# Kernel optimization log

Measured on AMD Instinct MI355X. Metric: run time of the kernel, lower is better.

## Reference

```python
import jax, jax.numpy as jnp
import numpy as np

KEY_DIM = 512
VAL_DIM = 512
BATCH = 32768
MEMORY_MAX_NORM = 5.0
TTT_LR_SCALE = 0.005
EPS = 1e-8


def setup_inputs() -> dict:
    key = jax.random.key(0)
    k1, k2, k3, k4, k5 = jax.random.split(key, 5)
    k = jax.random.normal(k1, (BATCH, KEY_DIM), dtype=jnp.float32)
    v = jax.random.normal(k2, (BATCH, VAL_DIM), dtype=jnp.float32)
    # memory weight init: normal(std=0.01)
    mem_w = jax.random.normal(k3, (VAL_DIM, KEY_DIM), dtype=jnp.float32) * 0.01
    # gate_proj: init is zeros/0.5; use small random weight + 0.5 bias for a
    # non-degenerate but realistic post-warmup state
    gate_w = jax.random.normal(k4, (3, KEY_DIM + VAL_DIM), dtype=jnp.float32) * 0.01
    gate_b = jnp.full((3,), 0.5, dtype=jnp.float32)
    momentum_S = jax.random.normal(k5, (VAL_DIM, KEY_DIM), dtype=jnp.float32) * 0.01
    return {"k": k, "v": v, "mem_w": mem_w, "gate_w": gate_w,
            "gate_b": gate_b, "momentum_S": momentum_S}


def _norm_clip(x, max_norm):
    n = jnp.linalg.norm(x)
    return jnp.where(n > max_norm, x * (max_norm / (n + EPS)), x)


def reference(k, v, mem_w, gate_w, gate_b, momentum_S):
    # retrieve: M(k) = k @ W^T ; loss = MSE(pred, v)
    retrieved = k @ mem_w.T                      # [B, val_dim]
    diff = retrieved - v
    loss = jnp.mean(diff * diff)

    # gates from batch-mean key/value
    kv_agg = jnp.concatenate([k.mean(0), v.mean(0)], axis=-1)  # [key+val]
    gates = jax.nn.sigmoid(kv_agg @ gate_w.T + gate_b)         # [3]
    alpha, eta, theta = gates[0], gates[1], gates[2]

    # analytic grad of MSE wrt W: 2/(B*val_dim) * (pred - v)^T @ k
    B, vd = diff.shape
    grad = (2.0 / (B * vd)) * (diff.T @ k)       # [val_dim, key_dim]
    grad_c = jnp.clip(grad, -1.0, 1.0)

    new_momentum = eta * momentum_S - TTT_LR_SCALE * theta * grad_c
    new_momentum = _norm_clip(new_momentum, MEMORY_MAX_NORM)

    new_weight = (1.0 - alpha) * mem_w + new_momentum
    new_weight = _norm_clip(new_weight, MEMORY_MAX_NORM)

    return retrieved, loss, new_weight, new_momentum, alpha, eta, theta
```

## Files before the change

### kernel.cpp

```cpp
#include <hip/hip_runtime.h>
#include <math.h>


typedef __bf16 bf16x8 __attribute__((ext_vector_type(8)));
typedef float f32x4 __attribute__((ext_vector_type(4)));
typedef float float4_t __attribute__((ext_vector_type(4)));
typedef unsigned short ushort4_t __attribute__((ext_vector_type(4)));
typedef unsigned short ushort8_t __attribute__((ext_vector_type(8)));

#define OUT_LOSS   16777216
#define OUT_W      16777217
#define OUT_MOM    17039361
#define OUT_ALPHA  17301505

#define OFF_GRAD   0u
#define OFF_CKP    1048576u
#define OFF_CVP    1572864u
#define OFF_LOSSP  2097152u
#define OFF_COLK   2105344u
#define OFF_COLV   2107392u
#define OFF_SCAL   2109440u
#define OFF_W16    2109504u
#define OFF_K16    2633792u
#define OFF_DIFF   36188224u
#define OFF_MRAW   OFF_K16
#define OFF_WRAW   (OFF_K16 + 1048576u)

__device__ __forceinline__ ushort4_t cvt4(float4_t v) {
  union { __bf16 b; unsigned short u; } c0, c1, c2, c3;
  c0.b = (__bf16)v.x; c1.b = (__bf16)v.y; c2.b = (__bf16)v.z; c3.b = (__bf16)v.w;
  ushort4_t h; h.x = c0.u; h.y = c1.u; h.z = c2.u; h.w = c3.u;
  return h;
}

__device__ __forceinline__ void gload_lds16(const unsigned short* g, unsigned short* l) {
  __builtin_amdgcn_global_load_lds(
      (const __attribute__((address_space(1))) unsigned int*)g,
      (__attribute__((address_space(3))) unsigned int*)l, 16, 0, 0);
}

__global__ __launch_bounds__(256) void k1_convert(
    const float* __restrict__ Kp, const float* __restrict__ Wp,
    unsigned short* __restrict__ k16, unsigned short* __restrict__ w16,
    float* __restrict__ colk_part)
{
  __shared__ float cp[512];
  const int t = threadIdx.x;
  const int cg = t & 127;
  const int g = t >> 7;
  const int b = blockIdx.x;
  if (b < 256) {
    const int r0 = b << 7;
    float p0 = 0.f, p1 = 0.f, p2 = 0.f, p3 = 0.f;
#pragma unroll 4
    for (int rr = g; rr < 128; rr += 2) {
      const size_t off = (size_t)(r0 + rr) * 512 + (cg << 2);
      const float4_t v = *reinterpret_cast<const float4_t*>(&Kp[off]);
      *reinterpret_cast<ushort4_t*>(&k16[off]) = cvt4(v);
      p0 += v.x; p1 += v.y; p2 += v.z; p3 += v.w;
    }
    if (g == 1) {
      cp[(cg << 2) + 0] = p0; cp[(cg << 2) + 1] = p1;
      cp[(cg << 2) + 2] = p2; cp[(cg << 2) + 3] = p3;
    }
    __syncthreads();
    if (g == 0) {
      colk_part[(size_t)b * 512 + (cg << 2) + 0] = p0 + cp[(cg << 2) + 0];
      colk_part[(size_t)b * 512 + (cg << 2) + 1] = p1 + cp[(cg << 2) + 1];
      colk_part[(size_t)b * 512 + (cg << 2) + 2] = p2 + cp[(cg << 2) + 2];
      colk_part[(size_t)b * 512 + (cg << 2) + 3] = p3 + cp[(cg << 2) + 3];
    }
  } else {
    const int r0 = (b - 256) << 5;
#pragma unroll 4
    for (int rr = g; rr < 32; rr += 2) {
      const size_t off = (size_t)(r0 + rr) * 512 + (cg << 2);
      const float4_t v = *reinterpret_cast<const float4_t*>(&Wp[off]);
      *reinterpret_cast<ushort4_t*>(&w16[off]) = cvt4(v);
    }
  }
}

__global__ __launch_bounds__(256) void k2_gemm(
    const unsigned short* __restrict__ k16, const unsigned short* __restrict__ w16,
    const float* __restrict__ Vp, float* __restrict__ outp,
    unsigned short* __restrict__ diff16,
    float* __restrict__ colv_part, float* __restrict__ loss_part)
{
  __shared__ __align__(16) unsigned short As[8192];
  __shared__ __align__(16) unsigned short Bs[4096];
  __shared__ float redc[128];
  __shared__ float redl[4];

  const int t = threadIdx.x, lane = t & 63, wv = t >> 6;
  const int tile = (blockIdx.x & 7) * 256 + (blockIdx.x >> 3);
  const int rt = tile >> 3, vt = tile & 7;
  const int row0 = rt << 7, vd0 = vt << 6;

  f32x4 acc[4][2];
#pragma unroll
  for (int m = 0; m < 4; ++m)
#pragma unroll
    for (int n = 0; n < 2; ++n)
      acc[m][n] = (f32x4){0.f, 0.f, 0.f, 0.f};

  const int srow = (wv << 3) + (lane >> 3);
  const int scol = (lane & 7) << 3;
  const unsigned short* pA = k16 + (size_t)(row0 + srow) * 512 + scol;
  const unsigned short* pB = w16 + (size_t)(vd0 + srow) * 512 + scol;
  unsigned short* lA = &As[wv << 9];
  unsigned short* lB = &Bs[wv << 9];

  const int fr = lane & 15, fq = lane >> 4;
  const int wr = (wv >> 1) << 6, wc = (wv & 1) << 5;

  for (int kk0 = 0; kk0 < 512; kk0 += 64) {
#pragma unroll
    for (int i = 0; i < 4; ++i)
      gload_lds16(pA + (i << 14) + kk0, lA + (i << 11));
#pragma unroll
    for (int i = 0; i < 2; ++i)
      gload_lds16(pB + (i << 14) + kk0, lB + (i << 11));
    __syncthreads();
#pragma unroll
    for (int kk = 0; kk < 64; kk += 32) {
      const int co = kk + (fq << 3);
      bf16x8 af[4], bfv[2];
#pragma unroll
      for (int m = 0; m < 4; ++m)
        af[m] = *reinterpret_cast<const bf16x8*>(&As[((wr + (m << 4) + fr) << 6) + co]);
#pragma unroll
      for (int n = 0; n < 2; ++n)
        bfv[n] = *reinterpret_cast<const bf16x8*>(&Bs[((wc + (n << 4) + fr) << 6) + co]);
#pragma unroll
      for (int m = 0; m < 4; ++m)
#pragma unroll
        for (int n = 0; n < 2; ++n)
          acc[m][n] = __builtin_amdgcn_mfma_f32_16x16x32_bf16(af[m], bfv[n], acc[m][n], 0, 0, 0);
    }
    __syncthreads();
  }

  float lsum = 0.f;
  float vcs[2] = {0.f, 0.f};
#pragma unroll
  for (int m = 0; m < 4; ++m) {
#pragma unroll
    for (int n = 0; n < 2; ++n) {
#pragma unroll
      for (int i = 0; i < 4; ++i) {
        const int rl = wr + (m << 4) + (fq << 2) + i;
        const int cl = wc + (n << 4) + fr;
        const size_t oi = (size_t)(row0 + rl) * 512 + vd0 + cl;
        const float rv = acc[m][n][i];
        outp[oi] = rv;
        const float vv = Vp[oi];
        const float d = rv - vv;
        lsum += d * d;
        vcs[n] += vv;
        union { __bf16 b; unsigned short u; } cd; cd.b = (__bf16)d;
        diff16[oi] = cd.u;
      }
    }
  }
#pragma unroll
  for (int o = 32; o; o >>= 1) lsum += __shfl_xor(lsum, o);
  if (lane == 0) redl[wv] = lsum;
#pragma unroll
  for (int n = 0; n < 2; ++n) {
    vcs[n] += __shfl_xor(vcs[n], 16);
    vcs[n] += __shfl_xor(vcs[n], 32);
  }
  if (fq == 0) {
#pragma unroll
    for (int n = 0; n < 2; ++n)
      redc[(wv << 5) + (n << 4) + fr] = vcs[n];
  }
  __syncthreads();
  if (t < 64) {
    const int h = t >> 5, lc = t & 31;
    colv_part[(size_t)rt * 512 + vd0 + t] =
        redc[(h << 5) + lc] + redc[((h + 2) << 5) + lc];
  }
  if (t == 0)
    loss_part[tile] = redl[0] + redl[1] + redl[2] + redl[3];
}

__global__ __launch_bounds__(256) void k3_grad(
    const unsigned short* __restrict__ diff16,
    const unsigned short* __restrict__ k16,
    float* __restrict__ grad)
{
  __shared__ __align__(16) unsigned short At[2][128][40];
  __shared__ __align__(16) unsigned short Bt[2][128][40];
  const int t = threadIdx.x;
  const int lane = t & 63;
  const int wv = t >> 6;
  const int b = blockIdx.x;
  const int x = b & 7;
  const int q = b >> 3;
  const int tile = q & 15;
  const int kc = ((q >> 4) << 3) | x;
  const int vd0 = (tile & 3) << 7;
  const int kd0 = (tile >> 2) << 7;
  const size_t r0 = (size_t)kc << 10;

  f32x4 acc[4][4];
#pragma unroll
  for (int m = 0; m < 4; ++m)
#pragma unroll
    for (int n = 0; n < 4; ++n)
      acc[m][n] = (f32x4){0.f, 0.f, 0.f, 0.f};

  const int dr = t >> 3;
  const int c0 = (t & 7) << 4;
  const int wr = (wv >> 1) << 6;
  const int wc = (wv & 1) << 6;
  const int fr = lane & 15;
  const int fq = lane >> 4;

  int cur = 0;
  for (int rr = 0; rr < 1024; rr += 32) {
    const size_t rowoff = (r0 + rr + dr) << 9;
    const ushort8_t a0 = *reinterpret_cast<const ushort8_t*>(&diff16[rowoff + vd0 + c0]);
    const ushort8_t a1 = *reinterpret_cast<const ushort8_t*>(&diff16[rowoff + vd0 + c0 + 8]);
    const ushort8_t b0 = *reinterpret_cast<const ushort8_t*>(&k16[rowoff + kd0 + c0]);
    const ushort8_t b1 = *reinterpret_cast<const ushort8_t*>(&k16[rowoff + kd0 + c0 + 8]);
    const int swz = ((c0 >> 4) & 3) << 3;
#pragma unroll
    for (int j = 0; j < 8; ++j) {
      const int drs = dr ^ swz;
      At[cur][c0 + j][drs] = a0[j];
      At[cur][c0 + 8 + j][drs] = a1[j];
      Bt[cur][c0 + j][drs] = b0[j];
      Bt[cur][c0 + 8 + j][drs] = b1[j];
    }
    __syncthreads();
    bf16x8 af[4], bfv[4];
#pragma unroll
    for (int m = 0; m < 4; ++m) {
      const int rA = wr + (m << 4) + fr;
      af[m] = *reinterpret_cast<const bf16x8*>(&At[cur][rA][(fq ^ ((rA >> 4) & 3)) << 3]);
    }
#pragma unroll
    for (int n = 0; n < 4; ++n) {
      const int rB = wc + (n << 4) + fr;
      bfv[n] = *reinterpret_cast<const bf16x8*>(&Bt[cur][rB][(fq ^ ((rB >> 4) & 3)) << 3]);
    }
#pragma unroll
    for (int m = 0; m < 4; ++m)
#pragma unroll
      for (int n = 0; n < 4; ++n)
        acc[m][n] = __builtin_amdgcn_mfma_f32_16x16x32_bf16(af[m], bfv[n], acc[m][n], 0, 0, 0);
    cur ^= 1;
  }
#pragma unroll
  for (int m = 0; m < 4; ++m)
#pragma unroll
    for (int n = 0; n < 4; ++n)
#pragma unroll
      for (int i = 0; i < 4; ++i)
        atomicAdd(&grad[(size_t)(vd0 + wr + (m << 4) + (fq << 2) + i) * 512
                        + kd0 + wc + (n << 4) + fr], acc[m][n][i]);
}

__global__ __launch_bounds__(256) void c1a_redcols(
    const float* __restrict__ ckp, const float* __restrict__ cvp,
    float* __restrict__ colk, float* __restrict__ colv)
{
  __shared__ float red[8][32];
  const int t = threadIdx.x, b = blockIdx.x;
  const int mtx = b >> 4;
  const int c = ((b & 15) << 5) + (t & 31);
  const int pg = t >> 5;
  const float* src = mtx ? cvp : ckp;
  float s = 0.f;
  for (int p = pg; p < 256; p += 8) s += src[(size_t)p * 512 + c];
  red[pg][t & 31] = s;
  __syncthreads();
  if (pg == 0) {
    float tot = 0.f;
#pragma unroll
    for (int j = 0; j < 8; ++j) tot += red[j][t & 31];
    (mtx ? colv : colk)[c] = tot;
  }
}

__global__ __launch_bounds__(256) void c1b_gates(
    const float* __restrict__ gw, const float* __restrict__ gb,
    const float* __restrict__ colk, const float* __restrict__ colv,
    const float* __restrict__ lossp, float* __restrict__ scal,
    float* __restrict__ outp)
{
  __shared__ float red3[3][4];
  __shared__ float redl[4];
  const int t = threadIdx.x, lane = t & 63, wvi = t >> 6;
  float p3[3] = {0.f, 0.f, 0.f};
  for (int j = t; j < 1024; j += 256) {
    const float kv = (j < 512 ? colk[j] : colv[j - 512]) * (1.0f / 32768.0f);
    p3[0] += kv * gw[j];
    p3[1] += kv * gw[1024 + j];
    p3[2] += kv * gw[2048 + j];
  }
  float ls = 0.f;
#pragma unroll
  for (int q = 0; q < 8; ++q) ls += lossp[t + (q << 8)];
#pragma unroll
  for (int o = 32; o; o >>= 1) {
    ls += __shfl_xor(ls, o);
#pragma unroll
    for (int g = 0; g < 3; ++g) p3[g] += __shfl_xor(p3[g], o);
  }
  if (lane == 0) {
    red3[0][wvi] = p3[0]; red3[1][wvi] = p3[1]; red3[2][wvi] = p3[2];
    redl[wvi] = ls;
  }
  __syncthreads();
  if (t == 0) {
    const float s0 = red3[0][0] + red3[0][1] + red3[0][2] + red3[0][3] + gb[0];
    const float s1 = red3[1][0] + red3[1][1] + red3[1][2] + red3[1][3] + gb[1];
    const float s2 = red3[2][0] + red3[2][1] + red3[2][2] + red3[2][3] + gb[2];
    const float alpha = 1.0f / (1.0f + expf(-s0));
    const float eta   = 1.0f / (1.0f + expf(-s1));
    const float theta = 1.0f / (1.0f + expf(-s2));
    scal[1] = 0.f; scal[2] = 0.f;
    scal[3] = alpha; scal[4] = eta; scal[5] = theta;
    outp[OUT_LOSS] = (redl[0] + redl[1] + redl[2] + redl[3]) * (1.0f / 16777216.0f);
    outp[OUT_ALPHA]     = alpha;
    outp[OUT_ALPHA + 1] = eta;
    outp[OUT_ALPHA + 2] = theta;
  }
}

__device__ __forceinline__ void block_atomic_sumsq(float sq, float* target) {
  __shared__ float red[4];
#pragma unroll
  for (int o = 32; o; o >>= 1) sq += __shfl_xor(sq, o);
  if ((threadIdx.x & 63) == 0) red[threadIdx.x >> 6] = sq;
  __syncthreads();
  if (threadIdx.x == 0) atomicAdd(target, red[0] + red[1] + red[2] + red[3]);
}

__global__ __launch_bounds__(256) void c2_mom(
    const float* __restrict__ grad, const float* __restrict__ S,
    float* scal, float* __restrict__ m_raw)
{
  const float eta = scal[4];
  const float cth = 0.005f * scal[5];
  const int i = ((blockIdx.x << 8) + threadIdx.x) << 2;
  const float4_t g = *reinterpret_cast<const float4_t*>(&grad[i]);
  const float4_t s = *reinterpret_cast<const float4_t*>(&S[i]);
  float4_t m; float sq = 0.f;
#pragma unroll
  for (int j = 0; j < 4; ++j) {
    float gj = g[j] * (2.0f / 16777216.0f);
    gj = fminf(1.0f, fmaxf(-1.0f, gj));
    m[j] = eta * s[j] - cth * gj;
    sq += m[j] * m[j];
  }
  *reinterpret_cast<float4_t*>(&m_raw[i]) = m;
  block_atomic_sumsq(sq, &scal[1]);
}

__global__ __launch_bounds__(256) void c3_wt(
    const float* __restrict__ m_raw, const float* __restrict__ memw,
    float* scal, float* __restrict__ w_raw, float* __restrict__ outp)
{
  const float nm = sqrtf(scal[1]);
  const float sm = nm > 5.0f ? 5.0f / (nm + 1e-8f) : 1.0f;
  const float oma = 1.0f - scal[3];
  const int i = ((blockIdx.x << 8) + threadIdx.x) << 2;
  const float4_t mr = *reinterpret_cast<const float4_t*>(&m_raw[i]);
  const float4_t wi = *reinterpret_cast<const float4_t*>(&memw[i]);
  float4_t w; float sq = 0.f;
#pragma unroll
  for (int j = 0; j < 4; ++j) {
    const float m = mr[j] * sm;
    outp[OUT_MOM + i + j] = m;
    w[j] = oma * wi[j] + m;
    sq += w[j] * w[j];
  }
  *reinterpret_cast<float4_t*>(&w_raw[i]) = w;
  block_atomic_sumsq(sq, &scal[2]);
}

__global__ __launch_bounds__(256) void c4_wt(
    const float* __restrict__ w_raw, const float* __restrict__ scal,
    float* __restrict__ outp)
{
  const float nw = sqrtf(scal[2]);
  const float sw = nw > 5.0f ? 5.0f / (nw + 1e-8f) : 1.0f;
  const int i = ((blockIdx.x << 8) + threadIdx.x) << 2;
  const float4_t w = *reinterpret_cast<const float4_t*>(&w_raw[i]);
#pragma unroll
  for (int j = 0; j < 4; ++j)
    outp[OUT_W + i + j] = w[j] * sw;
}

extern "C" void kernel_launch(void* const* d_in, const int* in_sizes, int n_in,
                              void* d_out, int out_size, void* d_ws, size_t ws_size,
                              hipStream_t stream)
{
  const float* Kp = (const float*)d_in[0];
  const float* Vp = (const float*)d_in[1];
  const float* Wp = (const float*)d_in[2];
  const float* GW = (const float*)d_in[3];
  const float* GB = (const float*)d_in[4];
  const float* Sp = (const float*)d_in[5];
  float* outp = (float*)d_out;
  char* ws = (char*)d_ws;

  float* grad            = (float*)(ws + OFF_GRAD);
  float* colk_part       = (float*)(ws + OFF_CKP);
  float* colv_part       = (float*)(ws + OFF_CVP);
  float* loss_part       = (float*)(ws + OFF_LOSSP);
  float* colk            = (float*)(ws + OFF_COLK);
  float* colv            = (float*)(ws + OFF_COLV);
  float* scal            = (float*)(ws + OFF_SCAL);
  unsigned short* w16    = (unsigned short*)(ws + OFF_W16);
  unsigned short* k16    = (unsigned short*)(ws + OFF_K16);
  unsigned short* diff16 = (unsigned short*)(ws + OFF_DIFF);
  float* m_raw           = (float*)(ws + OFF_MRAW);
  float* w_raw           = (float*)(ws + OFF_WRAW);

  hipMemsetAsync(ws + OFF_GRAD, 0, 1048576, stream);

  k1_convert<<<272, 256, 0, stream>>>(Kp, Wp, k16, w16, colk_part);
  k2_gemm<<<2048, 256, 0, stream>>>(k16, w16, Vp, outp, diff16, colv_part, loss_part);
  k3_grad<<<512, 256, 0, stream>>>(diff16, k16, grad);
  c1a_redcols<<<32, 256, 0, stream>>>(colk_part, colv_part, colk, colv);
  c1b_gates<<<1, 256, 0, stream>>>(GW, GB, colk, colv, loss_part, scal, outp);
  c2_mom<<<256, 256, 0, stream>>>(grad, Sp, scal, m_raw);
  c3_wt<<<256, 256, 0, stream>>>(m_raw, Wp, scal, w_raw, outp);
  c4_wt<<<256, 256, 0, stream>>>(w_raw, scal, outp);
}
```

Before: 173.6 us.

## Restructure forward GEMM: keep W slice resident in LDS, stream K from global

The forward k@W^T GEMM now uses 256x32 output tiles. Each block loads its full 32x512 bf16 slice of W into XOR-swizzled LDS once. The A operand (K) is read directly from global memory into registers instead of being staged through LDS, which removes the per-k-step barriers. The column-partial reduction is adjusted for the new row-tile count of 128 partials. The trade-off is heavier global traffic for K: each K row is re-read by 16 column tiles instead of 8, and fragments are loaded uncoalesced straight from global rather than shared via LDS.

```diff
diff --git a/kernel.cpp b/kernel.cpp
--- a/kernel.cpp
+++ b/kernel.cpp
@@ -31,12 +31,6 @@
   c0.b = (__bf16)v.x; c1.b = (__bf16)v.y; c2.b = (__bf16)v.z; c3.b = (__bf16)v.w;
   ushort4_t h; h.x = c0.u; h.y = c1.u; h.z = c2.u; h.w = c3.u;
   return h;
-}
-
-__device__ __forceinline__ void gload_lds16(const unsigned short* g, unsigned short* l) {
-  __builtin_amdgcn_global_load_lds(
-      (const __attribute__((address_space(1))) unsigned int*)g,
-      (__attribute__((address_space(3))) unsigned int*)l, 16, 0, 0);
 }
 
 __global__ __launch_bounds__(256) void k1_convert(
@@ -81,21 +75,32 @@
   }
 }
 
-__global__ __launch_bounds__(256) void k2_gemm(
+__global__ __launch_bounds__(256, 4) void k2_gemm(
     const unsigned short* __restrict__ k16, const unsigned short* __restrict__ w16,
     const float* __restrict__ Vp, float* __restrict__ outp,
     unsigned short* __restrict__ diff16,
     float* __restrict__ colv_part, float* __restrict__ loss_part)
 {
-  __shared__ __align__(16) unsigned short As[8192];
-  __shared__ __align__(16) unsigned short Bs[4096];
+  __shared__ __align__(16) unsigned short Bs[32 * 512];
   __shared__ float redc[128];
   __shared__ float redl[4];
 
   const int t = threadIdx.x, lane = t & 63, wv = t >> 6;
   const int tile = (blockIdx.x & 7) * 256 + (blockIdx.x >> 3);
-  const int rt = tile >> 3, vt = tile & 7;
-  const int row0 = rt << 7, vd0 = vt << 6;
+  const int rt = tile >> 4, vt = tile & 15;
+  const int row0 = rt << 8, vd0 = vt << 5;
+
+  {
+    const int c = t >> 3, p = t & 7;
+    const unsigned short* src = w16 + (size_t)(vd0 + c) * 512;
+#pragma unroll
+    for (int e = 0; e < 8; ++e) {
+      const int o = p + (e << 3);
+      const ushort8_t v = *reinterpret_cast<const ushort8_t*>(&src[o << 3]);
+      *reinterpret_cast<ushort8_t*>(&Bs[(c << 9) + ((o ^ (c & 7)) << 3)]) = v;
+    }
+  }
+  __syncthreads();
 
   f32x4 acc[4][2];
 #pragma unroll
@@ -104,41 +109,26 @@
     for (int n = 0; n < 2; ++n)
       acc[m][n] = (f32x4){0.f, 0.f, 0.f, 0.f};
 
-  const int srow = (wv << 3) + (lane >> 3);
-  const int scol = (lane & 7) << 3;
-  const unsigned short* pA = k16 + (size_t)(row0 + srow) * 512 + scol;
-  const unsigned short* pB = w16 + (size_t)(vd0 + srow) * 512 + scol;
-  unsigned short* lA = &As[wv << 9];
-  unsigned short* lB = &Bs[wv << 9];
-
   const int fr = lane & 15, fq = lane >> 4;
-  const int wr = (wv >> 1) << 6, wc = (wv & 1) << 5;
-
-  for (int kk0 = 0; kk0 < 512; kk0 += 64) {
-#pragma unroll
-    for (int i = 0; i < 4; ++i)
-      gload_lds16(pA + (i << 14) + kk0, lA + (i << 11));
-#pragma unroll
-    for (int i = 0; i < 2; ++i)
-      gload_lds16(pB + (i << 14) + kk0, lB + (i << 11));
-    __syncthreads();
-#pragma unroll
-    for (int kk = 0; kk < 64; kk += 32) {
-      const int co = kk + (fq << 3);
-      bf16x8 af[4], bfv[2];
-#pragma unroll
-      for (int m = 0; m < 4; ++m)
-        af[m] = *reinterpret_cast<const bf16x8*>(&As[((wr + (m << 4) + fr) << 6) + co]);
+  const unsigned short* pA = k16 + (size_t)(row0 + (wv << 6) + fr) * 512 + (fq << 3);
+
+#pragma unroll 4
+  for (int kb = 0; kb < 16; ++kb) {
+    bf16x8 af[4], bfv[2];
+#pragma unroll
+    for (int m = 0; m < 4; ++m)
+      af[m] = *reinterpret_cast<const bf16x8*>(&pA[(m << 13) + (kb << 5)]);
+#pragma unroll
+    for (int n = 0; n < 2; ++n) {
+      const int c = (n << 4) + fr;
+      const int s = ((kb << 2) + fq) ^ (c & 7);
+      bfv[n] = *reinterpret_cast<const bf16x8*>(&Bs[(c << 9) + (s << 3)]);
+    }
+#pragma unroll
+    for (int m = 0; m < 4; ++m)
 #pragma unroll
       for (int n = 0; n < 2; ++n)
-        bfv[n] = *reinterpret_cast<const bf16x8*>(&Bs[((wc + (n << 4) + fr) << 6) + co]);
-#pragma unroll
-      for (int m = 0; m < 4; ++m)
-#pragma unroll
-        for (int n = 0; n < 2; ++n)
-          acc[m][n] = __builtin_amdgcn_mfma_f32_16x16x32_bf16(af[m], bfv[n], acc[m][n], 0, 0, 0);
-    }
-    __syncthreads();
+        acc[m][n] = __builtin_amdgcn_mfma_f32_16x16x32_bf16(af[m], bfv[n], acc[m][n], 0, 0, 0);
   }
 
   float lsum = 0.f;
@@ -149,8 +139,8 @@
     for (int n = 0; n < 2; ++n) {
 #pragma unroll
       for (int i = 0; i < 4; ++i) {
-        const int rl = wr + (m << 4) + (fq << 2) + i;
-        const int cl = wc + (n << 4) + fr;
+        const int rl = (wv << 6) + (m << 4) + (fq << 2) + i;
+        const int cl = (n << 4) + fr;
         const size_t oi = (size_t)(row0 + rl) * 512 + vd0 + cl;
         const float rv = acc[m][n][i];
         outp[oi] = rv;
@@ -177,10 +167,9 @@
       redc[(wv << 5) + (n << 4) + fr] = vcs[n];
   }
   __syncthreads();
-  if (t < 64) {
-    const int h = t >> 5, lc = t & 31;
+  if (t < 32) {
     colv_part[(size_t)rt * 512 + vd0 + t] =
-        redc[(h << 5) + lc] + redc[((h + 2) << 5) + lc];
+        redc[t] + redc[32 + t] + redc[64 + t] + redc[96 + t];
   }
   if (t == 0)
     loss_part[tile] = redl[0] + redl[1] + redl[2] + redl[3];
@@ -274,8 +263,9 @@
   const int c = ((b & 15) << 5) + (t & 31);
   const int pg = t >> 5;
   const float* src = mtx ? cvp : ckp;
+  const int P = mtx ? 128 : 256;
   float s = 0.f;
-  for (int p = pg; p < 256; p += 8) s += src[(size_t)p * 512 + c];
+  for (int p = pg; p < P; p += 8) s += src[(size_t)p * 512 + c];
   red[pg][t & 31] = s;
   __syncthreads();
   if (pg == 0) {
```

New measurement: 212.1 us. 22.2% more time.

## Widen forward GEMM tile, prefetch grad loads, fold grad zeroing into convert

Applied to the files above, without the earlier changes.

The forward GEMM tile grows from 128x64 to 128x128 per block, halving the grid and raising MFMA work per LDS load. The gradient kernel now software-pipelines its global loads by fetching the next 32-row slab into registers while the current one is computed, hiding load latency. The separate memset of the gradient buffer is replaced by extra blocks in the convert kernel, removing one launch. The larger accumulator raises register pressure and may lower occupancy.

```diff
diff --git a/kernel.cpp b/kernel.cpp
--- a/kernel.cpp
+++ b/kernel.cpp
@@ -42,7 +42,7 @@
 __global__ __launch_bounds__(256) void k1_convert(
     const float* __restrict__ Kp, const float* __restrict__ Wp,
     unsigned short* __restrict__ k16, unsigned short* __restrict__ w16,
-    float* __restrict__ colk_part)
+    float* __restrict__ colk_part, float* __restrict__ grad)
 {
   __shared__ float cp[512];
   const int t = threadIdx.x;
@@ -70,7 +70,7 @@
       colk_part[(size_t)b * 512 + (cg << 2) + 2] = p2 + cp[(cg << 2) + 2];
       colk_part[(size_t)b * 512 + (cg << 2) + 3] = p3 + cp[(cg << 2) + 3];
     }
-  } else {
+  } else if (b < 272) {
     const int r0 = (b - 256) << 5;
 #pragma unroll 4
     for (int rr = g; rr < 32; rr += 2) {
@@ -78,6 +78,12 @@
       const float4_t v = *reinterpret_cast<const float4_t*>(&Wp[off]);
       *reinterpret_cast<ushort4_t*>(&w16[off]) = cvt4(v);
     }
+  } else {
+    const int base = (b - 272) << 14;
+    const float4_t z = (float4_t){0.f, 0.f, 0.f, 0.f};
+#pragma unroll
+    for (int j = 0; j < 16; ++j)
+      *reinterpret_cast<float4_t*>(&grad[base + (j << 10) + (t << 2)]) = z;
   }
 }
 
@@ -88,20 +94,20 @@
     float* __restrict__ colv_part, float* __restrict__ loss_part)
 {
   __shared__ __align__(16) unsigned short As[8192];
-  __shared__ __align__(16) unsigned short Bs[4096];
-  __shared__ float redc[128];
+  __shared__ __align__(16) unsigned short Bs[8192];
+  __shared__ float redc[256];
   __shared__ float redl[4];
 
   const int t = threadIdx.x, lane = t & 63, wv = t >> 6;
-  const int tile = (blockIdx.x & 7) * 256 + (blockIdx.x >> 3);
-  const int rt = tile >> 3, vt = tile & 7;
-  const int row0 = rt << 7, vd0 = vt << 6;
-
-  f32x4 acc[4][2];
+  const int tile = (blockIdx.x & 7) * 128 + (blockIdx.x >> 3);
+  const int rt = tile >> 2, vt = tile & 3;
+  const int row0 = rt << 7, vd0 = vt << 7;
+
+  f32x4 acc[4][4];
 #pragma unroll
   for (int m = 0; m < 4; ++m)
 #pragma unroll
-    for (int n = 0; n < 2; ++n)
+    for (int n = 0; n < 4; ++n)
       acc[m][n] = (f32x4){0.f, 0.f, 0.f, 0.f};
 
   const int srow = (wv << 3) + (lane >> 3);
@@ -112,46 +118,45 @@
   unsigned short* lB = &Bs[wv << 9];
 
   const int fr = lane & 15, fq = lane >> 4;
-  const int wr = (wv >> 1) << 6, wc = (wv & 1) << 5;
+  const int wr = (wv >> 1) << 6, wc = (wv & 1) << 6;
 
   for (int kk0 = 0; kk0 < 512; kk0 += 64) {
 #pragma unroll
-    for (int i = 0; i < 4; ++i)
+    for (int i = 0; i < 4; ++i) {
       gload_lds16(pA + (i << 14) + kk0, lA + (i << 11));
-#pragma unroll
-    for (int i = 0; i < 2; ++i)
       gload_lds16(pB + (i << 14) + kk0, lB + (i << 11));
+    }
     __syncthreads();
 #pragma unroll
     for (int kk = 0; kk < 64; kk += 32) {
       const int co = kk + (fq << 3);
-      bf16x8 af[4], bfv[2];
+      bf16x8 af[4], bfv[4];
 #pragma unroll
       for (int m = 0; m < 4; ++m)
         af[m] = *reinterpret_cast<const bf16x8*>(&As[((wr + (m << 4) + fr) << 6) + co]);
 #pragma unroll
-      for (int n = 0; n < 2; ++n)
+      for (int n = 0; n < 4; ++n)
         bfv[n] = *reinterpret_cast<const bf16x8*>(&Bs[((wc + (n << 4) + fr) << 6) + co]);
 #pragma unroll
       for (int m = 0; m < 4; ++m)
 #pragma unroll
-        for (int n = 0; n < 2; ++n)
+        for (int n = 0; n < 4; ++n)
           acc[m][n] = __builtin_amdgcn_mfma_f32_16x16x32_bf16(af[m], bfv[n], acc[m][n], 0, 0, 0);
     }
     __syncthreads();
   }
 
   float lsum = 0.f;
-  float vcs[2] = {0.f, 0.f};
+  float vcs[4] = {0.f, 0.f, 0.f, 0.f};
 #pragma unroll
   for (int m = 0; m < 4; ++m) {
 #pragma unroll
-    for (int n = 0; n < 2; ++n) {
+    for (int n = 0; n < 4; ++n) {
 #pragma unroll
       for (int i = 0; i < 4; ++i) {
-        const int rl = wr + (m << 4) + (fq << 2) + i;
-        const int cl = wc + (n << 4) + fr;
-        const size_t oi = (size_t)(row0 + rl) * 512 + vd0 + cl;
+        const int gr = row0 + wr + (m << 4) + (fq << 2) + i;
+        const int gc = vd0 + wc + (n << 4) + fr;
+        const size_t oi = (size_t)gr * 512 + gc;
         const float rv = acc[m][n][i];
         outp[oi] = rv;
         const float vv = Vp[oi];
@@ -167,20 +172,20 @@
   for (int o = 32; o; o >>= 1) lsum += __shfl_xor(lsum, o);
   if (lane == 0) redl[wv] = lsum;
 #pragma unroll
-  for (int n = 0; n < 2; ++n) {
+  for (int n = 0; n < 4; ++n) {
     vcs[n] += __shfl_xor(vcs[n], 16);
     vcs[n] += __shfl_xor(vcs[n], 32);
   }
   if (fq == 0) {
 #pragma unroll
-    for (int n = 0; n < 2; ++n)
-      redc[(wv << 5) + (n << 4) + fr] = vcs[n];
+    for (int n = 0; n < 4; ++n)
+      redc[(wv << 6) + (n << 4) + fr] = vcs[n];
   }
   __syncthreads();
-  if (t < 64) {
-    const int h = t >> 5, lc = t & 31;
+  if (t < 128) {
+    const int side = t >> 6, lc = t & 63;
     colv_part[(size_t)rt * 512 + vd0 + t] =
-        redc[(h << 5) + lc] + redc[((h + 2) << 5) + lc];
+        redc[side * 64 + lc] + redc[(side + 2) * 64 + lc];
   }
   if (t == 0)
     loss_part[tile] = redl[0] + redl[1] + redl[2] + redl[3];
@@ -218,23 +223,36 @@
   const int wc = (wv & 1) << 6;
   const int fr = lane & 15;
   const int fq = lane >> 4;
+  const int swz = ((c0 >> 4) & 3) << 3;
+  const int drs = dr ^ swz;
+
+  {
+    const size_t ro = (r0 + dr) << 9;
+  }
+  ushort8_t ca0, ca1, cb0, cb1;
+  {
+    const size_t ro = (r0 + dr) << 9;
+    ca0 = *reinterpret_cast<const ushort8_t*>(&diff16[ro + vd0 + c0]);
+    ca1 = *reinterpret_cast<const ushort8_t*>(&diff16[ro + vd0 + c0 + 8]);
+    cb0 = *reinterpret_cast<const ushort8_t*>(&k16[ro + kd0 + c0]);
+    cb1 = *reinterpret_cast<const ushort8_t*>(&k16[ro + kd0 + c0 + 8]);
+  }
 
   int cur = 0;
-  for (int rr = 0; rr < 1024; rr += 32) {
-    const size_t rowoff = (r0 + rr + dr) << 9;
-    const ushort8_t a0 = *reinterpret_cast<const ushort8_t*>(&diff16[rowoff + vd0 + c0]);
-    const ushort8_t a1 = *reinterpret_cast<const ushort8_t*>(&diff16[rowoff + vd0 + c0 + 8]);
-    const ushort8_t b0 = *reinterpret_cast<const ushort8_t*>(&k16[rowoff + kd0 + c0]);
-    const ushort8_t b1 = *reinterpret_cast<const ushort8_t*>(&k16[rowoff + kd0 + c0 + 8]);
-    const int swz = ((c0 >> 4) & 3) << 3;
+  for (int s = 0; s < 32; ++s) {
 #pragma unroll
     for (int j = 0; j < 8; ++j) {
-      const int drs = dr ^ swz;
-      At[cur][c0 + j][drs] = a0[j];
-      At[cur][c0 + 8 + j][drs] = a1[j];
-      Bt[cur][c0 + j][drs] = b0[j];
-      Bt[cur][c0 + 8 + j][drs] = b1[j];
-    }
+      At[cur][c0 + j][drs] = ca0[j];
+      At[cur][c0 + 8 + j][drs] = ca1[j];
+      Bt[cur][c0 + j][drs] = cb0[j];
+      Bt[cur][c0 + 8 + j][drs] = cb1[j];
+    }
+    const int rrn = (s < 31) ? ((s + 1) << 5) : 0;
+    const size_t ron = (r0 + rrn + dr) << 9;
+    const ushort8_t na0 = *reinterpret_cast<const ushort8_t*>(&diff16[ron + vd0 + c0]);
+    const ushort8_t na1 = *reinterpret_cast<const ushort8_t*>(&diff16[ron + vd0 + c0 + 8]);
+    const ushort8_t nb0 = *reinterpret_cast<const ushort8_t*>(&k16[ron + kd0 + c0]);
+    const ushort8_t nb1 = *reinterpret_cast<const ushort8_t*>(&k16[ron + kd0 + c0 + 8]);
     __syncthreads();
     bf16x8 af[4], bfv[4];
 #pragma unroll
@@ -252,6 +270,7 @@
 #pragma unroll
       for (int n = 0; n < 4; ++n)
         acc[m][n] = __builtin_amdgcn_mfma_f32_16x16x32_bf16(af[m], bfv[n], acc[m][n], 0, 0, 0);
+    ca0 = na0; ca1 = na1; cb0 = nb0; cb1 = nb1;
     cur ^= 1;
   }
 #pragma unroll
@@ -302,9 +321,7 @@
     p3[1] += kv * gw[1024 + j];
     p3[2] += kv * gw[2048 + j];
   }
-  float ls = 0.f;
-#pragma unroll
-  for (int q = 0; q < 8; ++q) ls += lossp[t + (q << 8)];
+  float ls = lossp[t] + lossp[256 + t] + lossp[512 + t] + lossp[768 + t];
 #pragma unroll
   for (int o = 32; o; o >>= 1) {
     ls += __shfl_xor(ls, o);
@@ -423,10 +440,8 @@
   float* m_raw           = (float*)(ws + OFF_MRAW);
   float* w_raw           = (float*)(ws + OFF_WRAW);
 
-  hipMemsetAsync(ws + OFF_GRAD, 0, 1048576, stream);
-
-  k1_convert<<<272, 256, 0, stream>>>(Kp, Wp, k16, w16, colk_part);
-  k2_gemm<<<2048, 256, 0, stream>>>(k16, w16, Vp, outp, diff16, colv_part, loss_part);
+  k1_convert<<<288, 256, 0, stream>>>(Kp, Wp, k16, w16, colk_part, grad);
+  k2_gemm<<<1024, 256, 0, stream>>>(k16, w16, Vp, outp, diff16, colv_part, loss_part);
   k3_grad<<<512, 256, 0, stream>>>(diff16, k16, grad);
   c1a_redcols<<<32, 256, 0, stream>>>(colk_part, colv_part, colk, colv);
   c1b_gates<<<1, 256, 0, stream>>>(GW, GB, colk, colv, loss_part, scal, outp);
```

Measured after the change: 167.9 us. 1.03x faster.
